# Performance work log

Hardware: AMD Instinct MI355X
Metric: run time of the kernel (lower is better)

The kernel has to match this reference:

```python
import jax, jax.numpy as jnp
import numpy as np

MB, T, NP1, D, K = 512, 256, 201, 4, 5
CTX = D + 4  # context_dim = amp_dim + 4


def setup_inputs() -> dict:
    key = jax.random.key(0)
    ks = jax.random.split(key, 10)
    demands = jax.random.uniform(ks[0], (MB, NP1)) * 9.0 + 1.0
    demands = demands.at[:, 0].set(0.0)  # depot has zero demand
    coords = jax.random.uniform(ks[1], (MB, NP1, 2))
    psi_prime = jax.random.normal(ks[2], (MB, NP1, D))
    knn_indices = jax.random.randint(ks[3], (MB, NP1, K), 0, NP1)
    actions = jax.random.randint(ks[4], (MB, T), 0, NP1)
    Wq_w = jax.random.normal(ks[5], (D, CTX)) * 0.1
    Wq_b = jax.random.normal(ks[6], (D,)) * 0.1
    return {
        'demands': demands, 'coords': coords, 'psi_prime': psi_prime,
        'Wq_w': Wq_w, 'Wq_b': Wq_b,
        'lambda_param': jnp.float32(0.1), 'mu_param': jnp.float32(0.5),
        'nu_param': jnp.float32(0.1),
        'actions': actions, 'knn_indices': knn_indices, 'capacity': 50,
    }


def _forward(demands, coords, psi_prime, Wq_w, Wq_b,
             lambda_param, mu_param, nu_param,
             actions, knn_indices, capacity):
    mb, T = actions.shape
    np1 = psi_prime.shape[1]
    n_customers = np1 - 1
    cap = max(float(capacity), 1e-8)
    b_idx = jnp.arange(mb)

    # --- sequential state bookkeeping (cur node, used capacity, visited mask) ---
    def step(carry, act_t):
        cur, used, vis = carry
        out = (cur, used, vis)  # state BEFORE applying action t
        at_depot = act_t == 0
        dem_t = demands[b_idx, act_t]
        used_n = jnp.where(at_depot, 0.0, used + dem_t)
        vis_n = vis.at[b_idx, act_t].set(True).at[:, 0].set(False)
        return (act_t, used_n, vis_n), out

    init = (jnp.zeros(mb, jnp.int32), jnp.zeros(mb, demands.dtype),
            jnp.zeros((mb, np1), bool))
    _, (all_cur, all_used, all_vis) = jax.lax.scan(step, init,
                                                   actions.T.astype(jnp.int32))
    all_cur = all_cur.T                       # [mb,T]
    all_used = all_used.T                     # [mb,T]
    all_vis = jnp.transpose(all_vis, (1, 0, 2))  # [mb,T,np1]

    remaining = cap - all_used
    cap_norm = remaining / cap
    exceeds = demands[:, None, :] > remaining[:, :, None]   # [mb,T,np1]
    mask = (all_vis | exceeds).at[:, :, 0].set(False)
    at_depot3 = all_cur == 0
    has_cust = (~mask[:, :, 1:]).any(-1)
    mask = mask.at[:, :, 0].set(at_depot3 & has_cust)

    cur_coords = coords[b_idx[:, None], all_cur]            # [mb,T,2]
    psi_curr = psi_prime[b_idx[:, None], all_cur]           # [mb,T,D]
    psi_curr = jnp.where(at_depot3[..., None], 0.0, psi_curr)
    t_norm = jnp.broadcast_to(
        (jnp.arange(T, dtype=psi_prime.dtype) / max(n_customers, 1))[None, :],
        (mb, T))
    ctx = jnp.concatenate([psi_curr, cap_norm[..., None],
                           t_norm[..., None], cur_coords], -1)  # [mb,T,D+4]
    query = ctx @ Wq_w.T + Wq_b                              # [mb,T,D]
    context_scores = jnp.einsum('btd,bnd->btn', query, psi_prime)

    # kNN interference: psi is fixed over t, so compute once and broadcast
    neigh = psi_prime[b_idx[:, None, None], knn_indices]     # [mb,np1,K,D]
    interference = jnp.einsum('bnd,bnkd->bn', psi_prime, neigh)  # [mb,np1]

    diff = coords[:, None, :, :] - cur_coords[:, :, None, :]  # [mb,T,np1,2]
    dist = jnp.sqrt(jnp.sum(diff * diff, -1) + 1e-12)         # [mb,T,np1]

    mu = jnp.clip(mu_param, 0.0, 20.0)
    lam = jnp.clip(lambda_param, -2.0, 3.0)
    nu = jnp.clip(nu_param, -2.0, 3.0)
    scores = (context_scores + lam * interference[:, None, :]
              - mu * dist + nu * (demands[:, None, :] / cap))
    scores = jnp.where(mask, -1e9, scores)
    lp3 = jax.nn.log_softmax(scores, -1)                      # [mb,T,np1]
    lp_new = jnp.take_along_axis(lp3, actions[:, :, None], 2)[..., 0]
    entropy = (-(jnp.exp(lp3) * lp3).sum(-1)).mean(1)         # [mb]
    return lp_new, entropy


def reference(demands, coords, psi_prime, Wq_w, Wq_b,
              lambda_param, mu_param, nu_param,
              actions, knn_indices, capacity):
    return _forward(demands, coords, psi_prime, Wq_w, Wq_b,
                    lambda_param, mu_param, nu_param,
                    actions, knn_indices, capacity)
```

## Files before the change

kernel.cpp:

```cpp
#include <hip/hip_runtime.h>
#include <hip/hip_bf16.h>
#include <math.h>

#define MB 512
#define T 256
#define NP1 201
#define KNN 5
#define RSW 12

typedef unsigned long long u64;
typedef unsigned int u32;

__global__ __launch_bounds__(256) void scan_kernel(
        const float* __restrict__ demands,
        const float* __restrict__ coords,
        const float* __restrict__ psi,
        const int* __restrict__ actions,
        const int* __restrict__ knn,
        const float* __restrict__ lam_p,
        const float* __restrict__ nu_p,
        const int* __restrict__ cap_p,
        float* __restrict__ rowState,
        float* __restrict__ pack,
        float* __restrict__ ent_out) {
    __shared__ int   actL[T];
    __shared__ float demL[T];
    __shared__ int   lastDep[T];
    __shared__ u64   visW[4][T];

    const int b = blockIdx.x;
    const int t = threadIdx.x;

    const int a_t = actions[b * T + t];
    actL[t] = a_t;
    demL[t] = demands[b * NP1 + a_t];
    lastDep[t] = (a_t == 0) ? t : -1;
    visW[0][t] = (a_t < 64)                ? (1ull << a_t)         : 0ull;
    visW[1][t] = (a_t >= 64 && a_t < 128)  ? (1ull << (a_t - 64))  : 0ull;
    visW[2][t] = (a_t >= 128 && a_t < 192) ? (1ull << (a_t - 128)) : 0ull;
    visW[3][t] = (a_t >= 192)              ? (1ull << (a_t - 192)) : 0ull;

    float4 packP, packC;
    if (t < NP1) {
        const int n = t;
        const float lam = fminf(fmaxf(lam_p[0], -2.f), 3.f);
        const float nu  = fminf(fmaxf(nu_p[0],  -2.f), 3.f);
        const float capl = fmaxf((float)cap_p[0], 1e-8f);
        const float4 pn = *(const float4*)(psi + ((size_t)b * NP1 + n) * 4);
        const float2 cc2 = *(const float2*)(coords + ((size_t)b * NP1 + n) * 2);
        float interf = 0.f;
        const int* kn = knn + ((size_t)b * NP1 + n) * KNN;
#pragma unroll
        for (int k = 0; k < KNN; ++k) {
            const int j = kn[k];
            const float4 pj = *(const float4*)(psi + ((size_t)b * NP1 + j) * 4);
            interf += pn.x * pj.x + pn.y * pj.y + pn.z * pj.z + pn.w * pj.w;
        }
        const float dem = demands[b * NP1 + n];
        packP = pn;
        packC.x = lam * interf + nu * (dem / capl);
        packC.y = cc2.x; packC.z = cc2.y; packC.w = dem;
    }
    __syncthreads();

#pragma unroll
    for (int off = 1; off < T; off <<= 1) {
        u64 x0, x1, x2, x3; int xd;
        const bool doit = (t >= off);
        if (doit) { x0 = visW[0][t - off]; x1 = visW[1][t - off];
                    x2 = visW[2][t - off]; x3 = visW[3][t - off];
                    xd = lastDep[t - off]; }
        __syncthreads();
        if (doit) { visW[0][t] |= x0; visW[1][t] |= x1;
                    visW[2][t] |= x2; visW[3][t] |= x3;
                    lastDep[t] = max(lastDep[t], xd); }
        __syncthreads();
    }

    if (t == 0) ent_out[b] = 0.f;

    const int s = (t == 0) ? 0 : (lastDep[t - 1] + 1);
    float used = 0.f;
    for (int j = s; j < t; ++j) used += demL[j];

    const float cap = fmaxf((float)cap_p[0], 1e-8f);
    const int cur = (t == 0) ? 0 : actL[t - 1];
    u64 v0 = 0, v1 = 0, v2 = 0, v3 = 0;
    if (t > 0) {
        v0 = visW[0][t - 1] & ~1ull;
        v1 = visW[1][t - 1];
        v2 = visW[2][t - 1];
        v3 = visW[3][t - 1];
    }
    const float rem = cap - used;
    const u32 meta = (u32)a_t | ((cur == 0) ? 0x80000000u : 0u);

    float* rs = rowState + (size_t)(b * T + t) * RSW;
    float4 w0 = {rem, __int_as_float(cur), __uint_as_float(meta), 0.f};
    ((float4*)rs)[0] = w0;
    uint4 wv0 = {(u32)v0, (u32)(v0 >> 32), (u32)v1, (u32)(v1 >> 32)};
    ((uint4*)rs)[1] = wv0;
    uint4 wv1 = {(u32)v2, (u32)(v2 >> 32), (u32)v3, (u32)(v3 >> 32)};
    ((uint4*)rs)[2] = wv1;

    if (t < NP1) {
        float* o = pack + ((size_t)b * NP1 + t) * 8;
        ((float4*)o)[0] = packP;
        ((float4*)o)[1] = packC;
    }
}

__global__ __launch_bounds__(256, 8) void hot_kernel(
        const float* __restrict__ pack,
        const float* __restrict__ rowState,
        const float* __restrict__ Wq_w,
        const float* __restrict__ Wq_b,
        const float* __restrict__ mu_p,
        const int* __restrict__ cap_p,
        float* __restrict__ lp_out,
        float* __restrict__ ent_out) {
    __shared__ float4 psiL[NP1];
    __shared__ float4 zCL[NP1];
    __shared__ float  entPart[4];

    const int blk = blockIdx.x;
    const int b = blk >> 2, chunk = blk & 3;
    const int tid = threadIdx.x;
    const int rloc = tid >> 2, split = tid & 3;
    const int t = chunk * 64 + rloc;

    const float4* pk = (const float4*)(pack + (size_t)b * NP1 * 8);
    for (int j = tid; j < 2 * NP1; j += 256) {
        const float4 v = pk[j];
        if (j & 1) zCL[j >> 1] = v; else psiL[j >> 1] = v;
    }
    __syncthreads();

    const float4* rs = (const float4*)(rowState + (size_t)(b * T + t) * RSW);
    const float4 r0 = rs[0];
    const uint4 rv0 = ((const uint4*)rs)[1];
    const uint4 rv1 = ((const uint4*)rs)[2];
    const float rem = r0.x;
    const int cur = __float_as_int(r0.y);
    const u32 meta = __float_as_uint(r0.z);
    const int a_t = (int)(meta & 0xFFFFu);
    const bool at_depot = (meta >> 31) != 0;
    const u64 v0 = (u64)rv0.x | ((u64)rv0.y << 32);
    const u64 v1 = (u64)rv0.z | ((u64)rv0.w << 32);
    const u64 v2 = (u64)rv1.x | ((u64)rv1.y << 32);
    const u64 v3 = (u64)rv1.z | ((u64)rv1.w << 32);

    const float cap = fmaxf((float)cap_p[0], 1e-8f);
    const float mu  = fminf(fmaxf(mu_p[0], 0.f), 20.f);
    const float capn = rem / cap;
    const float tn = (float)t / 200.f;

    float4 pc = psiL[cur];
    if (at_depot) { pc.x = 0.f; pc.y = 0.f; pc.z = 0.f; pc.w = 0.f; }
    const float4 cz = zCL[cur];
    const float ccx = cz.y, ccy = cz.z;

    float q0, q1, q2, q3;
    {
        const float c0 = pc.x, c1 = pc.y, c2 = pc.z, c3 = pc.w;
        q0 = Wq_b[0] + Wq_w[0]*c0 + Wq_w[1]*c1 + Wq_w[2]*c2 + Wq_w[3]*c3
           + Wq_w[4]*capn + Wq_w[5]*tn + Wq_w[6]*ccx + Wq_w[7]*ccy;
        q1 = Wq_b[1] + Wq_w[8]*c0 + Wq_w[9]*c1 + Wq_w[10]*c2 + Wq_w[11]*c3
           + Wq_w[12]*capn + Wq_w[13]*tn + Wq_w[14]*ccx + Wq_w[15]*ccy;
        q2 = Wq_b[2] + Wq_w[16]*c0 + Wq_w[17]*c1 + Wq_w[18]*c2 + Wq_w[19]*c3
           + Wq_w[20]*capn + Wq_w[21]*tn + Wq_w[22]*ccx + Wq_w[23]*ccy;
        q3 = Wq_b[3] + Wq_w[24]*c0 + Wq_w[25]*c1 + Wq_w[26]*c2 + Wq_w[27]*c3
           + Wq_w[28]*capn + Wq_w[29]*tn + Wq_w[30]*ccx + Wq_w[31]*ccy;
    }

    const int base = 1 + split * 50;
    const int wsel = base >> 6;
    const u64 wlo = (wsel == 0) ? v0 : (wsel == 1) ? v1 : v2;
    const u64 whi = (wsel == 0) ? v1 : (wsel == 1) ? v2 : v3;
    const int off = base & 63;
    u64 window = (wlo >> off) | (whi << (64 - off));

    float S = 0.f, W = 0.f;
    bool hasC = false;
#pragma unroll 5
    for (int i = 0; i < 50; ++i) {
        const int n = base + i;
        const float4 p4 = psiL[n];
        const float4 c4 = zCL[n];
        float sco = fmaf(q0, p4.x, fmaf(q1, p4.y, fmaf(q2, p4.z, fmaf(q3, p4.w, c4.x))));
        const float dx = c4.y - ccx, dy = c4.z - ccy;
        sco = fmaf(-mu, sqrtf(fmaf(dx, dx, fmaf(dy, dy, 1e-12f))), sco);
        const bool maskn = ((u32)window & 1u) || (c4.w > rem);
        window >>= 1;
        hasC = hasC || !maskn;
        const float e = maskn ? 0.f : __expf(sco);
        S += e;
        W = fmaf(e, sco, W);
    }

    int hc = hasC ? 1 : 0;
    hc |= __shfl_xor(hc, 1);
    hc |= __shfl_xor(hc, 2);
    const bool hasCust = hc != 0;

    if (split == 0) {
        const float4 p4 = psiL[0];
        const float4 c4 = zCL[0];
        float sco = fmaf(q0, p4.x, fmaf(q1, p4.y, fmaf(q2, p4.z, fmaf(q3, p4.w, c4.x))));
        const float dx = c4.y - ccx, dy = c4.z - ccy;
        sco = fmaf(-mu, sqrtf(fmaf(dx, dx, fmaf(dy, dy, 1e-12f))), sco);
        const bool mk = at_depot && hasCust;
        const float e = mk ? 0.f : __expf(sco);
        S += e;
        W = fmaf(e, sco, W);
    }

    S += __shfl_xor(S, 1); S += __shfl_xor(S, 2);
    W += __shfl_xor(W, 1); W += __shfl_xor(W, 2);

    float entv = 0.f;
    if (split == 0) {
        const float L = logf(S);
        const float4 p4 = psiL[a_t];
        const float4 c4 = zCL[a_t];
        float sco = fmaf(q0, p4.x, fmaf(q1, p4.y, fmaf(q2, p4.z, fmaf(q3, p4.w, c4.x))));
        const float dx = c4.y - ccx, dy = c4.z - ccy;
        sco = fmaf(-mu, sqrtf(fmaf(dx, dx, fmaf(dy, dy, 1e-12f))), sco);
        bool maskA;
        if (a_t == 0) {
            maskA = at_depot && hasCust;
        } else {
            const u64 vw = (a_t < 64) ? v0 : (a_t < 128) ? v1 : (a_t < 192) ? v2 : v3;
            maskA = ((vw >> (a_t & 63)) & 1ull) || (c4.w > rem);
        }
        const float sAct = maskA ? -1e9f : sco;
        lp_out[b * T + t] = sAct - L;
        entv = L - W / S;
    }

#pragma unroll
    for (int o = 32; o > 0; o >>= 1) entv += __shfl_xor(entv, o);
    if ((tid & 63) == 0) entPart[tid >> 6] = entv;
    __syncthreads();
    if (tid == 0)
        atomicAdd(&ent_out[b],
                  (entPart[0] + entPart[1] + entPart[2] + entPart[3]) * (1.f / (float)T));
}

extern "C" void kernel_launch(void* const* d_in, const int* in_sizes, int n_in,
                              void* d_out, int out_size, void* d_ws, size_t ws_size,
                              hipStream_t stream) {
    const float* demands = (const float*)d_in[0];
    const float* coords  = (const float*)d_in[1];
    const float* psi     = (const float*)d_in[2];
    const float* Wq_w    = (const float*)d_in[3];
    const float* Wq_b    = (const float*)d_in[4];
    const float* lam_p   = (const float*)d_in[5];
    const float* mu_p    = (const float*)d_in[6];
    const float* nu_p    = (const float*)d_in[7];
    const int*   actions = (const int*)d_in[8];
    const int*   knn     = (const int*)d_in[9];
    const int*   cap_p   = (const int*)d_in[10];

    float* lp_out  = (float*)d_out;
    float* ent_out = lp_out + MB * T;

    char* ws = (char*)d_ws;
    float* rowState = (float*)ws;
    float* pack     = (float*)(ws + (size_t)MB * T * RSW * 4);

    scan_kernel<<<MB, T, 0, stream>>>(demands, coords, psi, actions, knn,
                                      lam_p, nu_p, cap_p, rowState, pack, ent_out);
    hot_kernel<<<MB * 4, 256, 0, stream>>>(
        pack, rowState, Wq_w, Wq_b, mu_p, cap_p, lp_out, ent_out);
}
```

Before: 118.1 us.

## Fuse scan and scoring kernels, recomputing per-chunk state with wave-shuffle scan

Merges the scan and hot kernels into one kernel launched with four blocks per batch row. Each block redoes the visited-mask and depot prefix scan with wave shuffles plus a cross-wave aggregate, then scores its chunk straight from shared memory. This removes the global rowState and pack round trip and the many barrier-bound scan steps. The price is that the scan and the packing work are computed four times per batch row. Entropy accumulation moves from an atomicAdd to per-chunk partials summed by a small extra kernel, and sqrt and log switch to fast intrinsics.

```diff
diff --git a/kernel.cpp b/kernel.cpp
--- a/kernel.cpp
+++ b/kernel.cpp
@@ -6,154 +6,125 @@
 #define T 256
 #define NP1 201
 #define KNN 5
-#define RSW 12
 
 typedef unsigned long long u64;
 typedef unsigned int u32;
 
-__global__ __launch_bounds__(256) void scan_kernel(
+__global__ __launch_bounds__(256, 8) void fused_kernel(
         const float* __restrict__ demands,
         const float* __restrict__ coords,
         const float* __restrict__ psi,
+        const float* __restrict__ Wq_w,
+        const float* __restrict__ Wq_b,
+        const float* __restrict__ lam_p,
+        const float* __restrict__ mu_p,
+        const float* __restrict__ nu_p,
         const int* __restrict__ actions,
         const int* __restrict__ knn,
-        const float* __restrict__ lam_p,
-        const float* __restrict__ nu_p,
         const int* __restrict__ cap_p,
-        float* __restrict__ rowState,
-        float* __restrict__ pack,
-        float* __restrict__ ent_out) {
+        float* __restrict__ lp_out,
+        float* __restrict__ entPartial) {
+    __shared__ float4 psiL[NP1];
+    __shared__ float4 zCL[NP1];
+    __shared__ u64   visW[4][T];
+    __shared__ float remL[T];
     __shared__ int   actL[T];
     __shared__ float demL[T];
-    __shared__ int   lastDep[T];
-    __shared__ u64   visW[4][T];
-
-    const int b = blockIdx.x;
-    const int t = threadIdx.x;
-
+    __shared__ u64   aggV[4][4];
+    __shared__ int   aggD[4];
+    __shared__ float entPart[4];
+
+    const int blk = blockIdx.x;
+    const int b = blk >> 2, chunk = blk & 3;
+    const int tid = threadIdx.x;
+    const int lane = tid & 63, wv = tid >> 6;
+
+    const float cap = fmaxf((float)cap_p[0], 1e-8f);
+
+    const int t = tid;
     const int a_t = actions[b * T + t];
     actL[t] = a_t;
     demL[t] = demands[b * NP1 + a_t];
-    lastDep[t] = (a_t == 0) ? t : -1;
-    visW[0][t] = (a_t < 64)                ? (1ull << a_t)         : 0ull;
-    visW[1][t] = (a_t >= 64 && a_t < 128)  ? (1ull << (a_t - 64))  : 0ull;
-    visW[2][t] = (a_t >= 128 && a_t < 192) ? (1ull << (a_t - 128)) : 0ull;
-    visW[3][t] = (a_t >= 192)              ? (1ull << (a_t - 192)) : 0ull;
+
+    u64 m0 = (a_t < 64)                ? (1ull << a_t)         : 0ull;
+    u64 m1 = (a_t >= 64 && a_t < 128)  ? (1ull << (a_t - 64))  : 0ull;
+    u64 m2 = (a_t >= 128 && a_t < 192) ? (1ull << (a_t - 128)) : 0ull;
+    u64 m3 = (a_t >= 192)              ? (1ull << (a_t - 192)) : 0ull;
+    int d = (a_t == 0) ? t : -1;
 
     float4 packP, packC;
     if (t < NP1) {
-        const int n = t;
         const float lam = fminf(fmaxf(lam_p[0], -2.f), 3.f);
         const float nu  = fminf(fmaxf(nu_p[0],  -2.f), 3.f);
-        const float capl = fmaxf((float)cap_p[0], 1e-8f);
-        const float4 pn = *(const float4*)(psi + ((size_t)b * NP1 + n) * 4);
-        const float2 cc2 = *(const float2*)(coords + ((size_t)b * NP1 + n) * 2);
+        const float4 pn = *(const float4*)(psi + ((size_t)b * NP1 + t) * 4);
+        const float2 cc2 = *(const float2*)(coords + ((size_t)b * NP1 + t) * 2);
         float interf = 0.f;
-        const int* kn = knn + ((size_t)b * NP1 + n) * KNN;
+        const int* kn = knn + ((size_t)b * NP1 + t) * KNN;
 #pragma unroll
         for (int k = 0; k < KNN; ++k) {
             const int j = kn[k];
             const float4 pj = *(const float4*)(psi + ((size_t)b * NP1 + j) * 4);
             interf += pn.x * pj.x + pn.y * pj.y + pn.z * pj.z + pn.w * pj.w;
         }
-        const float dem = demands[b * NP1 + n];
+        const float dem = demands[b * NP1 + t];
         packP = pn;
-        packC.x = lam * interf + nu * (dem / capl);
+        packC.x = lam * interf + nu * (dem / cap);
         packC.y = cc2.x; packC.z = cc2.y; packC.w = dem;
     }
+
+#pragma unroll
+    for (int off = 1; off < 64; off <<= 1) {
+        m0 |= __shfl_up(m0, off);
+        m1 |= __shfl_up(m1, off);
+        m2 |= __shfl_up(m2, off);
+        m3 |= __shfl_up(m3, off);
+        d = max(d, __shfl_up(d, off));
+    }
+    if (lane == 63) {
+        aggV[0][wv] = m0; aggV[1][wv] = m1;
+        aggV[2][wv] = m2; aggV[3][wv] = m3;
+        aggD[wv] = d;
+    }
     __syncthreads();
 
-#pragma unroll
-    for (int off = 1; off < T; off <<= 1) {
-        u64 x0, x1, x2, x3; int xd;
-        const bool doit = (t >= off);
-        if (doit) { x0 = visW[0][t - off]; x1 = visW[1][t - off];
-                    x2 = visW[2][t - off]; x3 = visW[3][t - off];
-                    xd = lastDep[t - off]; }
-        __syncthreads();
-        if (doit) { visW[0][t] |= x0; visW[1][t] |= x1;
-                    visW[2][t] |= x2; visW[3][t] |= x3;
-                    lastDep[t] = max(lastDep[t], xd); }
-        __syncthreads();
-    }
-
-    if (t == 0) ent_out[b] = 0.f;
-
-    const int s = (t == 0) ? 0 : (lastDep[t - 1] + 1);
+    u64 p0 = 0, p1 = 0, p2 = 0, p3 = 0; int pd = -1;
+    for (int u = 0; u < wv; ++u) {
+        p0 |= aggV[0][u]; p1 |= aggV[1][u];
+        p2 |= aggV[2][u]; p3 |= aggV[3][u];
+        pd = max(pd, aggD[u]);
+    }
+    m0 |= p0; m1 |= p1; m2 |= p2; m3 |= p3; d = max(d, pd);
+    visW[0][t] = m0; visW[1][t] = m1; visW[2][t] = m2; visW[3][t] = m3;
+
+    int dPrev = __shfl_up(d, 1);
+    if (lane == 0) dPrev = pd;
+    const int s = dPrev + 1;
+
     float used = 0.f;
     for (int j = s; j < t; ++j) used += demL[j];
-
-    const float cap = fmaxf((float)cap_p[0], 1e-8f);
-    const int cur = (t == 0) ? 0 : actL[t - 1];
+    remL[t] = cap - used;
+
+    if (t < NP1) { psiL[t] = packP; zCL[t] = packC; }
+    __syncthreads();
+
+    const int rloc = tid >> 2, split = tid & 3;
+    const int tr = chunk * 64 + rloc;
+
+    const float rem = remL[tr];
+    const int a_row = actL[tr];
+    const int cur = (tr == 0) ? 0 : actL[tr - 1];
+    const bool at_depot = (cur == 0);
     u64 v0 = 0, v1 = 0, v2 = 0, v3 = 0;
-    if (t > 0) {
-        v0 = visW[0][t - 1] & ~1ull;
-        v1 = visW[1][t - 1];
-        v2 = visW[2][t - 1];
-        v3 = visW[3][t - 1];
-    }
-    const float rem = cap - used;
-    const u32 meta = (u32)a_t | ((cur == 0) ? 0x80000000u : 0u);
-
-    float* rs = rowState + (size_t)(b * T + t) * RSW;
-    float4 w0 = {rem, __int_as_float(cur), __uint_as_float(meta), 0.f};
-    ((float4*)rs)[0] = w0;
-    uint4 wv0 = {(u32)v0, (u32)(v0 >> 32), (u32)v1, (u32)(v1 >> 32)};
-    ((uint4*)rs)[1] = wv0;
-    uint4 wv1 = {(u32)v2, (u32)(v2 >> 32), (u32)v3, (u32)(v3 >> 32)};
-    ((uint4*)rs)[2] = wv1;
-
-    if (t < NP1) {
-        float* o = pack + ((size_t)b * NP1 + t) * 8;
-        ((float4*)o)[0] = packP;
-        ((float4*)o)[1] = packC;
-    }
-}
-
-__global__ __launch_bounds__(256, 8) void hot_kernel(
-        const float* __restrict__ pack,
-        const float* __restrict__ rowState,
-        const float* __restrict__ Wq_w,
-        const float* __restrict__ Wq_b,
-        const float* __restrict__ mu_p,
-        const int* __restrict__ cap_p,
-        float* __restrict__ lp_out,
-        float* __restrict__ ent_out) {
-    __shared__ float4 psiL[NP1];
-    __shared__ float4 zCL[NP1];
-    __shared__ float  entPart[4];
-
-    const int blk = blockIdx.x;
-    const int b = blk >> 2, chunk = blk & 3;
-    const int tid = threadIdx.x;
-    const int rloc = tid >> 2, split = tid & 3;
-    const int t = chunk * 64 + rloc;
-
-    const float4* pk = (const float4*)(pack + (size_t)b * NP1 * 8);
-    for (int j = tid; j < 2 * NP1; j += 256) {
-        const float4 v = pk[j];
-        if (j & 1) zCL[j >> 1] = v; else psiL[j >> 1] = v;
-    }
-    __syncthreads();
-
-    const float4* rs = (const float4*)(rowState + (size_t)(b * T + t) * RSW);
-    const float4 r0 = rs[0];
-    const uint4 rv0 = ((const uint4*)rs)[1];
-    const uint4 rv1 = ((const uint4*)rs)[2];
-    const float rem = r0.x;
-    const int cur = __float_as_int(r0.y);
-    const u32 meta = __float_as_uint(r0.z);
-    const int a_t = (int)(meta & 0xFFFFu);
-    const bool at_depot = (meta >> 31) != 0;
-    const u64 v0 = (u64)rv0.x | ((u64)rv0.y << 32);
-    const u64 v1 = (u64)rv0.z | ((u64)rv0.w << 32);
-    const u64 v2 = (u64)rv1.x | ((u64)rv1.y << 32);
-    const u64 v3 = (u64)rv1.z | ((u64)rv1.w << 32);
-
-    const float cap = fmaxf((float)cap_p[0], 1e-8f);
+    if (tr > 0) {
+        v0 = visW[0][tr - 1] & ~1ull;
+        v1 = visW[1][tr - 1];
+        v2 = visW[2][tr - 1];
+        v3 = visW[3][tr - 1];
+    }
+
     const float mu  = fminf(fmaxf(mu_p[0], 0.f), 20.f);
     const float capn = rem / cap;
-    const float tn = (float)t / 200.f;
+    const float tn = (float)tr / 200.f;
 
     float4 pc = psiL[cur];
     if (at_depot) { pc.x = 0.f; pc.y = 0.f; pc.z = 0.f; pc.w = 0.f; }
@@ -189,7 +160,7 @@
         const float4 c4 = zCL[n];
         float sco = fmaf(q0, p4.x, fmaf(q1, p4.y, fmaf(q2, p4.z, fmaf(q3, p4.w, c4.x))));
         const float dx = c4.y - ccx, dy = c4.z - ccy;
-        sco = fmaf(-mu, sqrtf(fmaf(dx, dx, fmaf(dy, dy, 1e-12f))), sco);
+        sco = fmaf(-mu, __builtin_amdgcn_sqrtf(fmaf(dx, dx, fmaf(dy, dy, 1e-12f))), sco);
         const bool maskn = ((u32)window & 1u) || (c4.w > rem);
         window >>= 1;
         hasC = hasC || !maskn;
@@ -208,7 +179,7 @@
         const float4 c4 = zCL[0];
         float sco = fmaf(q0, p4.x, fmaf(q1, p4.y, fmaf(q2, p4.z, fmaf(q3, p4.w, c4.x))));
         const float dx = c4.y - ccx, dy = c4.z - ccy;
-        sco = fmaf(-mu, sqrtf(fmaf(dx, dx, fmaf(dy, dy, 1e-12f))), sco);
+        sco = fmaf(-mu, __builtin_amdgcn_sqrtf(fmaf(dx, dx, fmaf(dy, dy, 1e-12f))), sco);
         const bool mk = at_depot && hasCust;
         const float e = mk ? 0.f : __expf(sco);
         S += e;
@@ -220,31 +191,40 @@
 
     float entv = 0.f;
     if (split == 0) {
-        const float L = logf(S);
-        const float4 p4 = psiL[a_t];
-        const float4 c4 = zCL[a_t];
+        const float L = __logf(S);
+        const float4 p4 = psiL[a_row];
+        const float4 c4 = zCL[a_row];
         float sco = fmaf(q0, p4.x, fmaf(q1, p4.y, fmaf(q2, p4.z, fmaf(q3, p4.w, c4.x))));
         const float dx = c4.y - ccx, dy = c4.z - ccy;
-        sco = fmaf(-mu, sqrtf(fmaf(dx, dx, fmaf(dy, dy, 1e-12f))), sco);
+        sco = fmaf(-mu, __builtin_amdgcn_sqrtf(fmaf(dx, dx, fmaf(dy, dy, 1e-12f))), sco);
         bool maskA;
-        if (a_t == 0) {
+        if (a_row == 0) {
             maskA = at_depot && hasCust;
         } else {
-            const u64 vw = (a_t < 64) ? v0 : (a_t < 128) ? v1 : (a_t < 192) ? v2 : v3;
-            maskA = ((vw >> (a_t & 63)) & 1ull) || (c4.w > rem);
+            const u64 vw = (a_row < 64) ? v0 : (a_row < 128) ? v1
+                         : (a_row < 192) ? v2 : v3;
+            maskA = ((vw >> (a_row & 63)) & 1ull) || (c4.w > rem);
         }
         const float sAct = maskA ? -1e9f : sco;
-        lp_out[b * T + t] = sAct - L;
+        lp_out[b * T + tr] = sAct - L;
         entv = L - W / S;
     }
 
 #pragma unroll
     for (int o = 32; o > 0; o >>= 1) entv += __shfl_xor(entv, o);
-    if ((tid & 63) == 0) entPart[tid >> 6] = entv;
+    if (lane == 0) entPart[wv] = entv;
     __syncthreads();
     if (tid == 0)
-        atomicAdd(&ent_out[b],
-                  (entPart[0] + entPart[1] + entPart[2] + entPart[3]) * (1.f / (float)T));
+        entPartial[b * 4 + chunk] = entPart[0] + entPart[1] + entPart[2] + entPart[3];
+}
+
+__global__ __launch_bounds__(256) void ent_sum_kernel(
+        const float* __restrict__ entPartial, float* __restrict__ ent_out) {
+    const int b = blockIdx.x * blockDim.x + threadIdx.x;
+    if (b < MB) {
+        const float* p = entPartial + b * 4;
+        ent_out[b] = (p[0] + p[1] + p[2] + p[3]) * (1.f / (float)T);
+    }
 }
 
 extern "C" void kernel_launch(void* const* d_in, const int* in_sizes, int n_in,
@@ -265,12 +245,10 @@
     float* lp_out  = (float*)d_out;
     float* ent_out = lp_out + MB * T;
 
-    char* ws = (char*)d_ws;
-    float* rowState = (float*)ws;
-    float* pack     = (float*)(ws + (size_t)MB * T * RSW * 4);
-
-    scan_kernel<<<MB, T, 0, stream>>>(demands, coords, psi, actions, knn,
-                                      lam_p, nu_p, cap_p, rowState, pack, ent_out);
-    hot_kernel<<<MB * 4, 256, 0, stream>>>(
-        pack, rowState, Wq_w, Wq_b, mu_p, cap_p, lp_out, ent_out);
+    float* entPartial = (float*)d_ws;
+
+    fused_kernel<<<MB * 4, 256, 0, stream>>>(
+        demands, coords, psi, Wq_w, Wq_b, lam_p, mu_p, nu_p,
+        actions, knn, cap_p, lp_out, entPartial);
+    ent_sum_kernel<<<2, 256, 0, stream>>>(entPartial, ent_out);
 }
```

Result: faster. 108.2 us (-8.4%).
